# Performance work log

Measured on AMD Instinct MI355X. Metric: run time of the kernel, lower is better.

## Reference

```python
import jax, jax.numpy as jnp
import numpy as np

N_NODES = 100000


def setup_inputs() -> dict:
    key = jax.random.key(0)
    k1, k2, k3 = jax.random.split(key, 3)
    x = jax.random.normal(k1, (N_NODES, 64), dtype=jnp.float32)
    edge_index = jax.random.randint(k2, (2, 1250000), 0, N_NODES, dtype=jnp.int64)
    W = jax.random.normal(k3, (128, 64), dtype=jnp.float32) * (1.0 / np.sqrt(128.0))
    b = jnp.zeros((64,), dtype=jnp.float32)
    return {"x": x, "edge_index": edge_index, "W": W, "b": b}


def reference(x, edge_index, W, b):
    n = x.shape[0]
    row, col = edge_index[0], edge_index[1]
    # scatter-add neighbor features onto destination nodes
    neigh = jax.ops.segment_sum(x[row], col, num_segments=n)          # [n, d]
    count = jax.ops.segment_sum(jnp.ones_like(col, dtype=x.dtype), col, num_segments=n)
    count = jnp.where(count == 0, jnp.asarray(1.0, x.dtype), count)   # avoid div-by-zero
    neigh = neigh / count[:, None]                                    # mean aggregation
    x_aggr = jnp.concatenate([x, neigh], axis=-1)                     # [n, 2d]
    out = x_aggr @ W + b                                              # [n, out_dim]
    return jax.nn.relu(out)  # dropout=0.0 (eval) -> identity
```

## Files before the change

kernel.cpp:

```cpp
#include <hip/hip_runtime.h>

#define D 64
#define NPB 64
#define THREADS 512
#define CAP 64
#define NFILL 2048

typedef int v4i __attribute__((ext_vector_type(4)));
typedef short bf16x8 __attribute__((ext_vector_type(8)));
typedef float f32x4 __attribute__((ext_vector_type(4)));

__device__ __forceinline__ unsigned short f2bf(float f) {
  unsigned u = __float_as_uint(f);
  return (unsigned short)((u + 0x7FFFu + ((u >> 16) & 1u)) >> 16);
}
__device__ __forceinline__ float bf2f(unsigned short h) {
  return __uint_as_float(((unsigned)h) << 16);
}
__device__ __forceinline__ void bfsplit(float v, unsigned short& hi, unsigned short& lo) {
  unsigned u = __float_as_uint(v);
  hi = (unsigned short)(u >> 16);
  float r = v - __uint_as_float(u & 0xFFFF0000u);
  lo = f2bf(r);
}

__global__ __launch_bounds__(256) void fill_prep_kernel(
    const int* __restrict__ ei, int* __restrict__ cnt,
    int* __restrict__ bucket, int e, int qpc,
    const float* __restrict__ x, ushort* __restrict__ xh,
    const float* __restrict__ W, ushort* __restrict__ wth,
    ushort* __restrict__ wtl, int n, int total4) {
  if (blockIdx.x < NFILL) {
    const int myx = blockIdx.x & 7;
    const int chunk = blockIdx.x >> 3;
    const int quads = e >> 2;
    const v4i* row4 = (const v4i*)ei;
    const v4i* col4 = (const v4i*)(ei + e);
    int qend = chunk * qpc + qpc;
    if (qend > quads) qend = quads;
    for (int q = chunk * qpc + threadIdx.x; q < qend; q += 256) {
      v4i r = __builtin_nontemporal_load(&row4[q]);
      v4i c = __builtin_nontemporal_load(&col4[q]);
      if (((c.x >> 11) & 7) == myx) {
        int p = atomicAdd(&cnt[c.x], 1);
        if (p < CAP) bucket[(size_t)c.x * CAP + p] = r.x * D;
      }
      if (((c.y >> 11) & 7) == myx) {
        int p = atomicAdd(&cnt[c.y], 1);
        if (p < CAP) bucket[(size_t)c.y * CAP + p] = r.y * D;
      }
      if (((c.z >> 11) & 7) == myx) {
        int p = atomicAdd(&cnt[c.z], 1);
        if (p < CAP) bucket[(size_t)c.z * CAP + p] = r.z * D;
      }
      if (((c.w >> 11) & 7) == myx) {
        int p = atomicAdd(&cnt[c.w], 1);
        if (p < CAP) bucket[(size_t)c.w * CAP + p] = r.w * D;
      }
    }
  } else {
    int t = (blockIdx.x - NFILL) * 256 + threadIdx.x;
    int nth = (gridDim.x - NFILL) * 256;
    for (int i = t; i < 2 * D * D; i += nth) {
      int nn = i >> 7, k = i & 127;
      float v = W[k * D + nn];
      unsigned short hi, lo;
      bfsplit(v, hi, lo);
      wth[i] = hi;
      wtl[i] = lo;
    }
    for (int i = t; i < total4; i += nth) {
      float4 v = ((const float4*)x)[i];
      ushort4 h;
      h.x = f2bf(v.x); h.y = f2bf(v.y); h.z = f2bf(v.z); h.w = f2bf(v.w);
      ((ushort4*)xh)[i] = h;
    }
  }
}

__global__ __launch_bounds__(THREADS, 8) void fused_bf_kernel(
    const float* __restrict__ x, const ushort* __restrict__ xh,
    const int* __restrict__ cnt,
    const ushort* __restrict__ wth, const ushort* __restrict__ wtl,
    const float* __restrict__ b, float* __restrict__ out,
    int n, int ntiles, int* __restrict__ tctr) {
  __shared__ __align__(16) ushort xsh[NPB * 128];
  __shared__ __align__(16) ushort xsl[NPB * 128];
  __shared__ int s_tile;

  const int lane = threadIdx.x & 63;
  const int wid  = threadIdx.x >> 6;
  const int* bucket = (const int*)out;
  const ushort* xpl = xh + lane;

  const int mt   = wid >> 1;
  const int nb   = (wid & 1) * 32;
  const int lrow = lane & 15;
  const int kgrp = (lane >> 4) * 8;
  const int arow = mt * 16 + lrow;
  const int aswz = (arow & 7) << 3;
  const int abase = arow * 128;
  const ushort* wh0 = wth + (nb + lrow) * 128;
  const ushort* wh1 = wth + (nb + 16 + lrow) * 128;
  const ushort* wl0 = wtl + (nb + lrow) * 128;
  const ushort* wl1 = wtl + (nb + 16 + lrow) * 128;
  const float bias0 = b[nb + lrow];
  const float bias1 = b[nb + 16 + lrow];
  const int drow = (lane >> 4) * 4;

  for (;;) {
    if (threadIdx.x == 0) s_tile = atomicAdd(tctr, 1);
    __syncthreads();
    const int tile = s_tile;
    if (tile >= ntiles) break;
    const int base = tile * NPB;

    {
      int node0 = base + wid * 8;
      int dgN = 0, bkN = 0;
      float xoN = 0.f;
      if (node0 < n) {
        dgN = cnt[node0];
        bkN = __builtin_nontemporal_load(&bucket[(size_t)node0 * CAP + lane]);
        xoN = __builtin_nontemporal_load(&x[(size_t)node0 * D + lane]);
      }
      for (int m = 0; m < 8; ++m) {
        int nl = wid * 8 + m;
        int node = base + nl;
        int dg = dgN, bk = bkN;
        float xown = xoN;
        if (m < 7) {
          int nq = node + 1;
          if (nq < n) {
            dgN = cnt[nq];
            bkN = __builtin_nontemporal_load(&bucket[(size_t)nq * CAP + lane]);
            xoN = __builtin_nontemporal_load(&x[(size_t)nq * D + lane]);
          } else {
            dgN = 0; bkN = 0; xoN = 0.f;
          }
        }
        int koff = nl * 128;
        int k0 = lane ^ ((nl & 7) << 3);
        if (node < n) {
          int dc = dg < CAP ? dg : CAP;
          float s0 = 0.f, s1 = 0.f, s2 = 0.f, s3 = 0.f;
          float s4 = 0.f, s5 = 0.f, s6 = 0.f, s7 = 0.f;
          int p = 0;
          for (; p + 8 <= dc; p += 8) {
            int a0 = __shfl(bk, p),     a1 = __shfl(bk, p + 1);
            int a2 = __shfl(bk, p + 2), a3 = __shfl(bk, p + 3);
            int a4 = __shfl(bk, p + 4), a5 = __shfl(bk, p + 5);
            int a6 = __shfl(bk, p + 6), a7 = __shfl(bk, p + 7);
            s0 += bf2f(xpl[a0]); s1 += bf2f(xpl[a1]);
            s2 += bf2f(xpl[a2]); s3 += bf2f(xpl[a3]);
            s4 += bf2f(xpl[a4]); s5 += bf2f(xpl[a5]);
            s6 += bf2f(xpl[a6]); s7 += bf2f(xpl[a7]);
          }
          for (; p + 4 <= dc; p += 4) {
            int a0 = __shfl(bk, p),     a1 = __shfl(bk, p + 1);
            int a2 = __shfl(bk, p + 2), a3 = __shfl(bk, p + 3);
            s0 += bf2f(xpl[a0]); s1 += bf2f(xpl[a1]);
            s2 += bf2f(xpl[a2]); s3 += bf2f(xpl[a3]);
          }
          for (; p < dc; ++p)
            s0 += bf2f(xpl[__shfl(bk, p)]);
          float sum = ((s0 + s1) + (s2 + s3)) + ((s4 + s5) + (s6 + s7));
          float inv = (dg > 0) ? (1.0f / (float)dg) : 0.0f;
          float mean = sum * inv;
          unsigned short h, l;
          bfsplit(xown, h, l);
          xsh[koff + k0] = h;       xsl[koff + k0] = l;
          bfsplit(mean, h, l);
          xsh[koff + 64 + k0] = h;  xsl[koff + 64 + k0] = l;
        } else {
          xsh[koff + k0] = 0;       xsl[koff + k0] = 0;
          xsh[koff + 64 + k0] = 0;  xsl[koff + 64 + k0] = 0;
        }
      }
    }
    __syncthreads();

    f32x4 acc0 = {bias0, bias0, bias0, bias0};
    f32x4 acc1 = {bias1, bias1, bias1, bias1};
#pragma unroll 2
    for (int ks = 0; ks < 4; ++ks) {
      int kb = ks * 32 + kgrp;
      int ke = abase + (kb ^ aswz);
      bf16x8 ah = *(const bf16x8*)&xsh[ke];
      bf16x8 al = *(const bf16x8*)&xsl[ke];
      bf16x8 w0h = *(const bf16x8*)(wh0 + kb);
      bf16x8 w1h = *(const bf16x8*)(wh1 + kb);
      acc0 = __builtin_amdgcn_mfma_f32_16x16x32_bf16(ah, w0h, acc0, 0, 0, 0);
      acc1 = __builtin_amdgcn_mfma_f32_16x16x32_bf16(ah, w1h, acc1, 0, 0, 0);
      acc0 = __builtin_amdgcn_mfma_f32_16x16x32_bf16(al, w0h, acc0, 0, 0, 0);
      acc1 = __builtin_amdgcn_mfma_f32_16x16x32_bf16(al, w1h, acc1, 0, 0, 0);
      bf16x8 w0l = *(const bf16x8*)(wl0 + kb);
      bf16x8 w1l = *(const bf16x8*)(wl1 + kb);
      acc0 = __builtin_amdgcn_mfma_f32_16x16x32_bf16(ah, w0l, acc0, 0, 0, 0);
      acc1 = __builtin_amdgcn_mfma_f32_16x16x32_bf16(ah, w1l, acc1, 0, 0, 0);
    }

#pragma unroll
    for (int r = 0; r < 4; ++r) {
      int node = base + mt * 16 + drow + r;
      if (node < n) {
        __builtin_nontemporal_store(fmaxf(acc0[r], 0.0f),
                                    &out[(size_t)node * D + nb + lrow]);
        __builtin_nontemporal_store(fmaxf(acc1[r], 0.0f),
                                    &out[(size_t)node * D + nb + 16 + lrow]);
      }
    }
    __syncthreads();
  }
}

__global__ __launch_bounds__(256) void fill_cap_kernel(
    const int* __restrict__ ei, int* __restrict__ cnt,
    int* __restrict__ bucket, int e) {
  int t = blockIdx.x * blockDim.x + threadIdx.x;
  if (t * 4 >= e) return;
  int4 r4 = ((const int4*)ei)[t];
  int4 c4 = ((const int4*)(ei + e))[t];
  int p0 = atomicAdd(&cnt[c4.x], 1);
  int p1 = atomicAdd(&cnt[c4.y], 1);
  int p2 = atomicAdd(&cnt[c4.z], 1);
  int p3 = atomicAdd(&cnt[c4.w], 1);
  if (p0 < CAP) bucket[(size_t)c4.x * CAP + p0] = r4.x;
  if (p1 < CAP) bucket[(size_t)c4.y * CAP + p1] = r4.y;
  if (p2 < CAP) bucket[(size_t)c4.z * CAP + p2] = r4.z;
  if (p3 < CAP) bucket[(size_t)c4.w * CAP + p3] = r4.w;
}

__global__ __launch_bounds__(THREADS, 8) void fused_cap_kernel(
    const float* __restrict__ x, const int* __restrict__ cnt,
    const float* __restrict__ W, const float* __restrict__ b,
    float* __restrict__ out, int n) {
  __shared__ __align__(16) float xs[NPB * 128];
  const int lane = threadIdx.x & 63;
  const int wid  = threadIdx.x >> 6;
  const int base = blockIdx.x * NPB;
  const int* bucket = (const int*)out;

  for (int m = 0; m < 8; ++m) {
    int nl = wid * 8 + m;
    int node = base + nl;
    if (node < n) {
      int dg = cnt[node];
      int dc = dg < CAP ? dg : CAP;
      int bk = bucket[(size_t)node * CAP + lane];
      float xown = x[(size_t)node * D + lane];
      float s0 = 0.f, s1 = 0.f, s2 = 0.f, s3 = 0.f;
      int p = 0;
      for (; p + 4 <= dc; p += 4) {
        int a0 = __shfl(bk, p),     a1 = __shfl(bk, p + 1);
        int a2 = __shfl(bk, p + 2), a3 = __shfl(bk, p + 3);
        s0 += x[(size_t)a0 * D + lane];
        s1 += x[(size_t)a1 * D + lane];
        s2 += x[(size_t)a2 * D + lane];
        s3 += x[(size_t)a3 * D + lane];
      }
      for (; p < dc; ++p)
        s0 += x[(size_t)__shfl(bk, p) * D + lane];
      float sum = (s0 + s1) + (s2 + s3);
      float inv = (dg > 0) ? (1.0f / (float)dg) : 0.0f;
      xs[nl * 128 + lane]      = xown;
      xs[nl * 128 + 64 + lane] = sum * inv;
    } else {
      xs[nl * 128 + lane]      = 0.0f;
      xs[nl * 128 + 64 + lane] = 0.0f;
    }
  }
  __syncthreads();

  const int col = lane;
  float bias = b[col];
  float acc[8];
#pragma unroll
  for (int m = 0; m < 8; ++m) acc[m] = bias;
  for (int k = 0; k < 128; k += 4) {
    float w0 = W[(k + 0) * 64 + col];
    float w1 = W[(k + 1) * 64 + col];
    float w2 = W[(k + 2) * 64 + col];
    float w3 = W[(k + 3) * 64 + col];
#pragma unroll
    for (int m = 0; m < 8; ++m) {
      int nl = wid + m * 8;
      float4 xv = *(const float4*)&xs[nl * 128 + k];
      acc[m] = fmaf(xv.x, w0, acc[m]);
      acc[m] = fmaf(xv.y, w1, acc[m]);
      acc[m] = fmaf(xv.z, w2, acc[m]);
      acc[m] = fmaf(xv.w, w3, acc[m]);
    }
  }
#pragma unroll
  for (int m = 0; m < 8; ++m) {
    int node = base + wid + m * 8;
    if (node < n)
      out[(size_t)node * D + col] = fmaxf(acc[m], 0.0f);
  }
}

extern "C" void kernel_launch(void* const* d_in, const int* in_sizes, int n_in,
                              void* d_out, int out_size, void* d_ws, size_t ws_size,
                              hipStream_t stream) {
  const float* x = (const float*)d_in[0];
  const int* ei = (const int*)d_in[1];
  const float* W = (const float*)d_in[2];
  const float* b = (const float*)d_in[3];
  float* out = (float*)d_out;

  int n = in_sizes[0] / D;
  int e = in_sizes[1] / 2;
  int ntiles = (n + NPB - 1) / NPB;

  size_t xh_bytes = (size_t)n * D * sizeof(ushort);
  size_t cnt_off  = (xh_bytes + 255) & ~(size_t)255;
  size_t tctr_off = (cnt_off + (size_t)n * sizeof(int) + 255) & ~(size_t)255;
  size_t wth_off  = tctr_off + 256;
  size_t wtl_off  = wth_off + 2 * D * D * sizeof(ushort);
  size_t need     = wtl_off + 2 * D * D * sizeof(ushort) + 256;

  if (ws_size >= need && (e & 3) == 0 && n <= (1 << 17)) {
    ushort* xh  = (ushort*)d_ws;
    int* cnt    = (int*)((char*)d_ws + cnt_off);
    int* tctr   = (int*)((char*)d_ws + tctr_off);
    ushort* wth = (ushort*)((char*)d_ws + wth_off);
    ushort* wtl = (ushort*)((char*)d_ws + wtl_off);

    (void)hipMemsetAsync((char*)d_ws + cnt_off, 0,
                         tctr_off + 256 - cnt_off, stream);

    int total4 = n * D / 4;
    int quads = e >> 2;
    int qpc = (quads + 255) / 256;
    fill_prep_kernel<<<NFILL + 256, 256, 0, stream>>>(
        ei, cnt, (int*)d_out, e, qpc, x, xh, W, wth, wtl, n, total4);

    fused_bf_kernel<<<1024, THREADS, 0, stream>>>(
        x, xh, cnt, wth, wtl, b, out, n, ntiles, tctr);
  } else {
    int* cnt = (int*)d_ws;
    (void)hipMemsetAsync(cnt, 0, (size_t)n * sizeof(int), stream);
    int quads = e / 4;
    fill_cap_kernel<<<(quads + 255) / 256, 256, 0, stream>>>(ei, cnt, (int*)d_out, e);
    fused_cap_kernel<<<ntiles, THREADS, 0, stream>>>(x, cnt, W, b, out, n);
  }
}
```

Before: 222.9 us.

## Merge fill/prep and fused GEMM kernels into one persistent kernel with grid barriers

Combines the bucket-fill/bf16-conversion kernel and the fused aggregation+GEMM kernel into a single 1024-block persistent kernel separated by software grid barriers. Count zeroing moves into the kernel so the large memset shrinks to a tiny one for the sync counters. This is meant to remove the launch gap and the tail drain between kernels. The cost is two grid-wide spin barriers and a changed fill partition of 896 blocks with 512 threads. Correctness depends on all 1024 blocks being co-resident.

```diff
diff --git a/kernel.cpp b/kernel.cpp
--- a/kernel.cpp
+++ b/kernel.cpp
@@ -4,7 +4,8 @@
 #define NPB 64
 #define THREADS 512
 #define CAP 64
-#define NFILL 2048
+#define GRID 1024
+#define NFILLB 896
 
 typedef int v4i __attribute__((ext_vector_type(4)));
 typedef short bf16x8 __attribute__((ext_vector_type(8)));
@@ -24,44 +25,43 @@
   lo = f2bf(r);
 }
 
-__global__ __launch_bounds__(256) void fill_prep_kernel(
-    const int* __restrict__ ei, int* __restrict__ cnt,
-    int* __restrict__ bucket, int e, int qpc,
-    const float* __restrict__ x, ushort* __restrict__ xh,
-    const float* __restrict__ W, ushort* __restrict__ wth,
-    ushort* __restrict__ wtl, int n, int total4) {
-  if (blockIdx.x < NFILL) {
-    const int myx = blockIdx.x & 7;
-    const int chunk = blockIdx.x >> 3;
-    const int quads = e >> 2;
-    const v4i* row4 = (const v4i*)ei;
-    const v4i* col4 = (const v4i*)(ei + e);
-    int qend = chunk * qpc + qpc;
-    if (qend > quads) qend = quads;
-    for (int q = chunk * qpc + threadIdx.x; q < qend; q += 256) {
-      v4i r = __builtin_nontemporal_load(&row4[q]);
-      v4i c = __builtin_nontemporal_load(&col4[q]);
-      if (((c.x >> 11) & 7) == myx) {
-        int p = atomicAdd(&cnt[c.x], 1);
-        if (p < CAP) bucket[(size_t)c.x * CAP + p] = r.x * D;
-      }
-      if (((c.y >> 11) & 7) == myx) {
-        int p = atomicAdd(&cnt[c.y], 1);
-        if (p < CAP) bucket[(size_t)c.y * CAP + p] = r.y * D;
-      }
-      if (((c.z >> 11) & 7) == myx) {
-        int p = atomicAdd(&cnt[c.z], 1);
-        if (p < CAP) bucket[(size_t)c.z * CAP + p] = r.z * D;
-      }
-      if (((c.w >> 11) & 7) == myx) {
-        int p = atomicAdd(&cnt[c.w], 1);
-        if (p < CAP) bucket[(size_t)c.w * CAP + p] = r.w * D;
-      }
-    }
-  } else {
-    int t = (blockIdx.x - NFILL) * 256 + threadIdx.x;
-    int nth = (gridDim.x - NFILL) * 256;
-    for (int i = t; i < 2 * D * D; i += nth) {
+__device__ __forceinline__ void grid_barrier(int* bar) {
+  __syncthreads();
+  if (threadIdx.x == 0) {
+    __threadfence();
+    int ticket = __hip_atomic_fetch_add(bar, 1, __ATOMIC_ACQ_REL,
+                                        __HIP_MEMORY_SCOPE_AGENT);
+    int target = (ticket / GRID + 1) * GRID;
+    while (__hip_atomic_load(bar, __ATOMIC_ACQUIRE,
+                             __HIP_MEMORY_SCOPE_AGENT) < target)
+      __builtin_amdgcn_s_sleep(16);
+    __threadfence();
+  }
+  __syncthreads();
+}
+
+__global__ __launch_bounds__(THREADS, 8) void mega_kernel(
+    const float* __restrict__ x, const int* __restrict__ ei,
+    const float* __restrict__ W, const float* __restrict__ b,
+    float* __restrict__ out, ushort* __restrict__ xh,
+    int* __restrict__ cnt, int* __restrict__ sync_base,
+    ushort* __restrict__ wth, ushort* __restrict__ wtl,
+    int n, int e, int total4, int ntiles, int qpc) {
+  __shared__ __align__(16) ushort xsh[NPB * 128];
+  __shared__ __align__(16) ushort xsl[NPB * 128];
+  __shared__ int s_tile;
+
+  int* tctr = sync_base;
+  int* bar  = sync_base + 16;
+
+  const int lane = threadIdx.x & 63;
+  const int wid  = threadIdx.x >> 6;
+
+  {
+    int gt = blockIdx.x * THREADS + threadIdx.x;
+    int gn = GRID * THREADS;
+    for (int i = gt; i < n; i += gn) cnt[i] = 0;
+    for (int i = gt; i < 2 * D * D; i += gn) {
       int nn = i >> 7, k = i & 127;
       float v = W[k * D + nn];
       unsigned short hi, lo;
@@ -69,6 +69,41 @@
       wth[i] = hi;
       wtl[i] = lo;
     }
+  }
+  grid_barrier(bar);
+
+  if (blockIdx.x < NFILLB) {
+    const int myx = blockIdx.x & 7;
+    const int chunk = blockIdx.x >> 3;
+    const int quads = e >> 2;
+    const v4i* row4 = (const v4i*)ei;
+    const v4i* col4 = (const v4i*)(ei + e);
+    int* bucket = (int*)out;
+    int qend = chunk * qpc + qpc;
+    if (qend > quads) qend = quads;
+    for (int q = chunk * qpc + threadIdx.x; q < qend; q += THREADS) {
+      v4i r = __builtin_nontemporal_load(&row4[q]);
+      v4i c = __builtin_nontemporal_load(&col4[q]);
+      if (((c.x >> 11) & 7) == myx) {
+        int p = atomicAdd(&cnt[c.x], 1);
+        if (p < CAP) bucket[(size_t)c.x * CAP + p] = r.x * D;
+      }
+      if (((c.y >> 11) & 7) == myx) {
+        int p = atomicAdd(&cnt[c.y], 1);
+        if (p < CAP) bucket[(size_t)c.y * CAP + p] = r.y * D;
+      }
+      if (((c.z >> 11) & 7) == myx) {
+        int p = atomicAdd(&cnt[c.z], 1);
+        if (p < CAP) bucket[(size_t)c.z * CAP + p] = r.z * D;
+      }
+      if (((c.w >> 11) & 7) == myx) {
+        int p = atomicAdd(&cnt[c.w], 1);
+        if (p < CAP) bucket[(size_t)c.w * CAP + p] = r.w * D;
+      }
+    }
+  } else {
+    int t = (blockIdx.x - NFILLB) * THREADS + threadIdx.x;
+    int nth = (GRID - NFILLB) * THREADS;
     for (int i = t; i < total4; i += nth) {
       float4 v = ((const float4*)x)[i];
       ushort4 h;
@@ -76,20 +111,8 @@
       ((ushort4*)xh)[i] = h;
     }
   }
-}
-
-__global__ __launch_bounds__(THREADS, 8) void fused_bf_kernel(
-    const float* __restrict__ x, const ushort* __restrict__ xh,
-    const int* __restrict__ cnt,
-    const ushort* __restrict__ wth, const ushort* __restrict__ wtl,
-    const float* __restrict__ b, float* __restrict__ out,
-    int n, int ntiles, int* __restrict__ tctr) {
-  __shared__ __align__(16) ushort xsh[NPB * 128];
-  __shared__ __align__(16) ushort xsl[NPB * 128];
-  __shared__ int s_tile;
-
-  const int lane = threadIdx.x & 63;
-  const int wid  = threadIdx.x >> 6;
+  grid_barrier(bar);
+
   const int* bucket = (const int*)out;
   const ushort* xpl = xh + lane;
 
@@ -315,29 +338,28 @@
 
   size_t xh_bytes = (size_t)n * D * sizeof(ushort);
   size_t cnt_off  = (xh_bytes + 255) & ~(size_t)255;
-  size_t tctr_off = (cnt_off + (size_t)n * sizeof(int) + 255) & ~(size_t)255;
-  size_t wth_off  = tctr_off + 256;
+  size_t sync_off = (cnt_off + (size_t)n * sizeof(int) + 255) & ~(size_t)255;
+  size_t wth_off  = sync_off + 256;
   size_t wtl_off  = wth_off + 2 * D * D * sizeof(ushort);
   size_t need     = wtl_off + 2 * D * D * sizeof(ushort) + 256;
 
   if (ws_size >= need && (e & 3) == 0 && n <= (1 << 17)) {
-    ushort* xh  = (ushort*)d_ws;
-    int* cnt    = (int*)((char*)d_ws + cnt_off);
-    int* tctr   = (int*)((char*)d_ws + tctr_off);
-    ushort* wth = (ushort*)((char*)d_ws + wth_off);
-    ushort* wtl = (ushort*)((char*)d_ws + wtl_off);
-
-    (void)hipMemsetAsync((char*)d_ws + cnt_off, 0,
-                         tctr_off + 256 - cnt_off, stream);
+    ushort* xh   = (ushort*)d_ws;
+    int* cnt     = (int*)((char*)d_ws + cnt_off);
+    int* syncb   = (int*)((char*)d_ws + sync_off);
+    ushort* wth  = (ushort*)((char*)d_ws + wth_off);
+    ushort* wtl  = (ushort*)((char*)d_ws + wtl_off);
+
+    (void)hipMemsetAsync((char*)d_ws + sync_off, 0, 256, stream);
 
     int total4 = n * D / 4;
     int quads = e >> 2;
-    int qpc = (quads + 255) / 256;
-    fill_prep_kernel<<<NFILL + 256, 256, 0, stream>>>(
-        ei, cnt, (int*)d_out, e, qpc, x, xh, W, wth, wtl, n, total4);
-
-    fused_bf_kernel<<<1024, THREADS, 0, stream>>>(
-        x, xh, cnt, wth, wtl, b, out, n, ntiles, tctr);
+    int chunks = NFILLB / 8;
+    int qpc = (quads + chunks - 1) / chunks;
+
+    mega_kernel<<<GRID, THREADS, 0, stream>>>(
+        x, ei, W, b, out, xh, cnt, syncb, wth, wtl,
+        n, e, total4, ntiles, qpc);
   } else {
     int* cnt = (int*)d_ws;
     (void)hipMemsetAsync(cnt, 0, (size_t)n * sizeof(int), stream);
```

Measured after the change: 465.6 us. 109% more time.
